# Performance work log

Hardware: AMD Instinct MI355X
Metric: run time of the kernel (lower is better)

Reference implementation:

```python
import jax, jax.numpy as jnp
import numpy as np
from jax import lax

HEADS = 8
DIM_HEAD = 64
DIM = HEADS * DIM_HEAD  # 512


def _dwconv(x_nchw, w):
    # depthwise 3x3, stride 1, pad 1 (SAME), groups = channels
    return lax.conv_general_dilated(
        x_nchw, w, window_strides=(1, 1), padding='SAME',
        feature_group_count=x_nchw.shape[1],
        dimension_numbers=('NCHW', 'OIHW', 'NCHW'))


def setup_inputs() -> dict:
    key = jax.random.key(0)
    ks = jax.random.split(key, 9)
    b, h, w, c = 4, 256, 256, DIM
    s = 1.0 / np.sqrt(c)
    return {
        'x_in':    jax.random.normal(ks[0], (b, h, w, c), jnp.float32),
        'Wq':      jax.random.normal(ks[1], (c, DIM), jnp.float32) * s,
        'Wk':      jax.random.normal(ks[2], (c, DIM), jnp.float32) * s,
        'Wv':      jax.random.normal(ks[3], (c, DIM), jnp.float32) * s,
        'rescale': jnp.ones((HEADS, 1, 1), jnp.float32),
        'proj_w':  jax.random.normal(ks[4], (DIM, c), jnp.float32) * s,
        'proj_b':  jnp.zeros((c,), jnp.float32),
        'conv1_w': jax.random.normal(ks[5], (c, 1, 3, 3), jnp.float32) * (1.0 / 3.0),
        'conv2_w': jax.random.normal(ks[6], (c, 1, 3, 3), jnp.float32) * (1.0 / 3.0),
    }


def reference(x_in, Wq, Wk, Wv, rescale, proj_w, proj_b, conv1_w, conv2_w):
    b, h, w, c = x_in.shape
    n = h * w
    x = x_in.reshape(b, n, c)
    q_inp = x @ Wq  # [b, n, heads*d]
    k_inp = x @ Wk
    v_inp = x @ Wv

    def heads_dn(t):  # [b, n, heads*d] -> [b, heads, d, n]
        return t.reshape(b, n, HEADS, DIM_HEAD).transpose(0, 2, 3, 1)

    q = heads_dn(q_inp)
    k = heads_dn(k_inp)
    v = heads_dn(v_inp)

    # L2-normalize along token axis (F.normalize, eps=1e-12)
    qn = q / jnp.maximum(jnp.linalg.norm(q, axis=-1, keepdims=True), 1e-12)
    kn = k / jnp.maximum(jnp.linalg.norm(k, axis=-1, keepdims=True), 1e-12)

    # channel attention: [b, heads, d, d]
    attn = jnp.einsum('bhdn,bhen->bhde', kn, qn) * rescale
    attn = jax.nn.softmax(attn, axis=-1)
    xo = jnp.einsum('bhde,bhen->bhdn', attn, v)  # [b, heads, d, n]

    xo = xo.transpose(0, 3, 1, 2).reshape(b, n, HEADS * DIM_HEAD)
    out_c = (xo @ proj_w + proj_b).reshape(b, h, w, c)

    # depthwise conv positional embedding on v_inp
    vp = v_inp.reshape(b, h, w, c).transpose(0, 3, 1, 2)  # NCHW
    vp = _dwconv(vp, conv1_w)
    vp = jax.nn.gelu(vp, approximate=False)
    vp = _dwconv(vp, conv2_w)
    out_p = vp.transpose(0, 2, 3, 1)

    return out_c + out_p
```

## Files before the change

kernel.cpp:

```cpp
#include <hip/hip_runtime.h>
#include <math.h>

typedef unsigned short u16;
typedef unsigned int   u32;
typedef __attribute__((ext_vector_type(4))) float f32x4;
typedef __attribute__((ext_vector_type(8))) short bf16x8;
typedef __attribute__((ext_vector_type(8))) u16   u16x8;
typedef __attribute__((ext_vector_type(4))) u16   u16x4;

#define DEVI static __device__ __forceinline__

DEVI float bf2f(u16 a){ u32 u=((u32)a)<<16; float f; __builtin_memcpy(&f,&u,4); return f; }
DEVI u16 f2bf(float f){ u32 u; __builtin_memcpy(&u,&f,4); u=u+0x7fffu+((u>>16)&1u); return (u16)(u>>16); }

DEVI void gload16(const u16* src, u16* lds){
  __builtin_amdgcn_global_load_lds((const __attribute__((address_space(1))) u32*)src,
                                   (__attribute__((address_space(3))) u32*)lds, 16, 0, 0);
}

__global__ void k_wvt(const float* __restrict__ Wv, u16* __restrict__ WvT){
  int n = blockIdx.x;
  for (int k = threadIdx.x; k < 512; k += 256)
    WvT[(size_t)n*512 + k] = f2bf(Wv[(size_t)k*512 + n]);
}
__global__ void k_wrep(const float* __restrict__ w1, const float* __restrict__ w2, float* __restrict__ wt){
  int s = blockIdx.x/9, tap = blockIdx.x%9, c = threadIdx.x;
  const float* w = s ? w2 : w1;
  wt[(size_t)(s*9+tap)*512 + c] = w[(size_t)c*9 + tap];
}

__global__ __launch_bounds__(1024, 4) void k_gemm_v(const float* __restrict__ x, const u16* __restrict__ WvT,
                                                    u16* __restrict__ v, u16* __restrict__ xbT){
  __shared__ __align__(16) u16 Al[128*64];
  __shared__ __align__(16) u16 Bl[512*64];
  const int tid = threadIdx.x;
  const int l = tid & 63, w = tid >> 6;
  const int wr = w >> 3, wc = w & 7;
  const long r0 = (long)blockIdx.x * 128;
  f32x4 acc[4][4] = {};
  const int arow = tid >> 3, ac = tid & 7;
  const float* xp = x + (r0 + arow)*512 + ac*8;
  f32x4 va = *(const f32x4*)xp, vb = *(const f32x4*)(xp+4);
  for (int k0 = 0; k0 < 512; k0 += 64){
    {
      u16x8 o;
      o[0]=f2bf(va.x); o[1]=f2bf(va.y); o[2]=f2bf(va.z); o[3]=f2bf(va.w);
      o[4]=f2bf(vb.x); o[5]=f2bf(vb.y); o[6]=f2bf(vb.z); o[7]=f2bf(vb.w);
      *(u16x8*)&Al[arow*64 + ((ac ^ (arow&7))*8)] = o;
    }
    if (k0 < 448){
      va = *(const f32x4*)(xp + k0 + 64);
      vb = *(const f32x4*)(xp + k0 + 68);
    }
    #pragma unroll
    for (int i = 0; i < 4; ++i){
      int blkrow = w*32 + i*8;
      int r = blkrow + (l>>3);
      const u16* src = WvT + (size_t)r*512 + k0 + (((l&7) ^ ((l>>3)&7))*8);
      gload16(src, &Bl[blkrow*64]);
    }
    __syncthreads();
    #pragma unroll
    for (int ks = 0; ks < 2; ++ks){
      bf16x8 af[4], bfr[4];
      #pragma unroll
      for (int mf = 0; mf < 4; ++mf){
        int row = wr*64 + mf*16 + (l&15);
        af[mf] = *(const bf16x8*)&Al[row*64 + (((ks*4 + (l>>4)) ^ (row&7))*8)];
      }
      #pragma unroll
      for (int nf = 0; nf < 4; ++nf){
        int row = wc*64 + nf*16 + (l&15);
        bfr[nf] = *(const bf16x8*)&Bl[row*64 + (((ks*4 + (l>>4)) ^ (row&7))*8)];
      }
      #pragma unroll
      for (int mf = 0; mf < 4; ++mf)
        #pragma unroll
        for (int nf = 0; nf < 4; ++nf)
          acc[mf][nf] = __builtin_amdgcn_mfma_f32_16x16x32_bf16(af[mf], bfr[nf], acc[mf][nf], 0,0,0);
    }
    {
      int chloc = tid & 63, tg = tid >> 6;
      u16x8 o;
      #pragma unroll
      for (int j = 0; j < 8; ++j){
        int tok = tg*8 + j;
        o[j] = Al[tok*64 + (((chloc>>3) ^ (tok&7))*8) + (chloc&7)];
      }
      *(u16x8*)(xbT + (size_t)(k0 + chloc)*262144 + r0 + tg*8) = o;
    }
    __syncthreads();
  }
  #pragma unroll
  for (int mf = 0; mf < 4; ++mf)
    #pragma unroll
    for (int nf = 0; nf < 4; ++nf){
      int col = wc*64 + nf*16 + (l&15);
      #pragma unroll
      for (int j = 0; j < 4; ++j){
        long row = r0 + wr*64 + mf*16 + (l>>4)*4 + j;
        v[(size_t)row*512 + col] = f2bf(acc[mf][nf][j]);
      }
    }
}

__global__ __launch_bounds__(1024, 4) void k_syrk(const u16* __restrict__ xbT, float* __restrict__ P){
  __shared__ __align__(16) u16 AL[256*64];
  __shared__ __align__(16) u16 BL[256*64];
  const int bid = blockIdx.x;
  const int cs = bid & 63, combo = (bid>>6)%3, b = bid/192;
  const int hA = (combo==2) ? 1 : 0;
  const int tid = threadIdx.x;
  const int l = tid & 63, w = tid>>6, wi = w>>2, wj = w&3;
  const long tokb0 = (long)b*65536 + (long)cs*1024;
  const u16* Bread = (combo==1) ? BL : AL;
  f32x4 acc[4][4] = {};
  for (int st = 0; st < 16; ++st){
    const long tokb = tokb0 + st*64;
    #pragma unroll
    for (int i = 0; i < 2; ++i){
      int blkrow = w*16 + i*8;
      int r = blkrow + (l>>3);
      const u16* src = xbT + (size_t)(hA*256 + r)*262144 + tokb + (((l&7) ^ ((l>>3)&7))*8);
      gload16(src, &AL[blkrow*64]);
    }
    if (combo == 1){
      #pragma unroll
      for (int i = 0; i < 2; ++i){
        int blkrow = w*16 + i*8;
        int r = blkrow + (l>>3);
        const u16* src = xbT + (size_t)(256 + r)*262144 + tokb + (((l&7) ^ ((l>>3)&7))*8);
        gload16(src, &BL[blkrow*64]);
      }
    }
    __syncthreads();
    #pragma unroll
    for (int ks = 0; ks < 2; ++ks){
      bf16x8 af[4], bfr[4];
      #pragma unroll
      for (int mf = 0; mf < 4; ++mf){
        int row = wi*64 + mf*16 + (l&15);
        af[mf] = *(const bf16x8*)&AL[row*64 + (((ks*4 + (l>>4)) ^ (row&7))*8)];
      }
      #pragma unroll
      for (int nf = 0; nf < 4; ++nf){
        int row = wj*64 + nf*16 + (l&15);
        bfr[nf] = *(const bf16x8*)&Bread[row*64 + (((ks*4 + (l>>4)) ^ (row&7))*8)];
      }
      #pragma unroll
      for (int mf = 0; mf < 4; ++mf)
        #pragma unroll
        for (int nf = 0; nf < 4; ++nf)
          acc[mf][nf] = __builtin_amdgcn_mfma_f32_16x16x32_bf16(af[mf], bfr[nf], acc[mf][nf], 0,0,0);
    }
    __syncthreads();
  }
  float* Pb = P + (size_t)bid*65536;
  #pragma unroll
  for (int mf = 0; mf < 4; ++mf)
    #pragma unroll
    for (int nf = 0; nf < 4; ++nf)
      #pragma unroll
      for (int j = 0; j < 4; ++j){
        int il = wi*64 + mf*16 + (l>>4)*4 + j;
        int jl = wj*64 + nf*16 + (l&15);
        Pb[il*256 + jl] = acc[mf][nf][j];
      }
}

__global__ void k_sred(const float* __restrict__ P, float* __restrict__ S){
  int bid = blockIdx.x;
  int il = bid & 255, combo = (bid>>8)%3, b = bid/768;
  int hi = (combo==2)?1:0, hj = (combo==0)?0:1;
  int jl = threadIdx.x;
  float s = 0.f;
  for (int cs = 0; cs < 64; ++cs)
    s += P[((size_t)(b*192 + combo*64 + cs))*65536 + il*256 + jl];
  int I = hi*256 + il, J = hj*256 + jl;
  S[((size_t)b*512 + I)*512 + J] = s;
  if (combo == 1) S[((size_t)b*512 + J)*512 + I] = s;
}

__global__ __launch_bounds__(256) void k_a1(const float* __restrict__ S, const float* __restrict__ Wq,
                                            const float* __restrict__ Wk, float* __restrict__ T, float* __restrict__ U){
  int bid = blockIdx.x;
  int b = bid>>6, rem = bid&63, which = rem>>5, rbase = (rem&31)*16;
  const float* W = which ? Wk : Wq;
  float* O = which ? U : T;
  int tid = threadIdx.x;
  int rg = tid>>6, c0 = (tid&63)*8;
  const float* Sr = S + (size_t)b*262144 + (size_t)(rbase + rg*4)*512;
  float acc[4][8] = {};
  for (int k = 0; k < 512; ++k){
    float s0 = Sr[k], s1 = Sr[512+k], s2 = Sr[1024+k], s3 = Sr[1536+k];
    f32x4 wa = *(const f32x4*)(W + (size_t)k*512 + c0);
    f32x4 wb = *(const f32x4*)(W + (size_t)k*512 + c0 + 4);
    #pragma unroll
    for (int j = 0; j < 4; ++j){
      acc[0][j]   += s0*wa[j]; acc[1][j]   += s1*wa[j]; acc[2][j]   += s2*wa[j]; acc[3][j]   += s3*wa[j];
      acc[0][4+j] += s0*wb[j]; acc[1][4+j] += s1*wb[j]; acc[2][4+j] += s2*wb[j]; acc[3][4+j] += s3*wb[j];
    }
  }
  float* Ob = O + (size_t)b*262144;
  #pragma unroll
  for (int i = 0; i < 4; ++i){
    f32x4 o0, o1;
    o0.x=acc[i][0]; o0.y=acc[i][1]; o0.z=acc[i][2]; o0.w=acc[i][3];
    o1.x=acc[i][4]; o1.y=acc[i][5]; o1.z=acc[i][6]; o1.w=acc[i][7];
    *(f32x4*)(Ob + (size_t)(rbase+rg*4+i)*512 + c0)     = o0;
    *(f32x4*)(Ob + (size_t)(rbase+rg*4+i)*512 + c0 + 4) = o1;
  }
}

__global__ void k_a2(const float* __restrict__ Wq, const float* __restrict__ Wk,
                     const float* __restrict__ T, const float* __restrict__ U,
                     float* __restrict__ G, float* __restrict__ q2, float* __restrict__ k2){
  int b = blockIdx.x>>3, h = blockIdx.x&7;
  int tid = threadIdx.x;
  int d0 = (tid>>4)*4, e0 = (tid&15)*4;
  const float* Tb = T + (size_t)b*262144;
  float acc[4][4] = {};
  for (int i = 0; i < 512; ++i){
    f32x4 wk = *(const f32x4*)(Wk + (size_t)i*512 + h*64 + d0);
    f32x4 tv = *(const f32x4*)(Tb + (size_t)i*512 + h*64 + e0);
    #pragma unroll
    for (int di = 0; di < 4; ++di)
      #pragma unroll
      for (int ej = 0; ej < 4; ++ej) acc[di][ej] += wk[di]*tv[ej];
  }
  float* Gb = G + ((size_t)(b*8+h))*4096;
  #pragma unroll
  for (int di = 0; di < 4; ++di)
    #pragma unroll
    for (int ej = 0; ej < 4; ++ej) Gb[(d0+di)*64 + e0+ej] = acc[di][ej];
  if (tid < 64){
    int e = tid; float a = 0.f;
    for (int j = 0; j < 512; ++j) a += Wq[(size_t)j*512 + h*64 + e] * Tb[(size_t)j*512 + h*64 + e];
    q2[b*512 + h*64 + e] = a;
  } else if (tid < 128){
    int d = tid - 64; float a = 0.f;
    const float* Ub = U + (size_t)b*262144;
    for (int j = 0; j < 512; ++j) a += Wk[(size_t)j*512 + h*64 + d] * Ub[(size_t)j*512 + h*64 + d];
    k2[b*512 + h*64 + d] = a;
  }
}

__global__ void k_a3(const float* __restrict__ G, const float* __restrict__ resc,
                     const float* __restrict__ q2, const float* __restrict__ k2, float* __restrict__ Aa){
  int b = blockIdx.x>>3, h = blockIdx.x&7;
  int d = threadIdx.x;
  const float* g = G + ((size_t)(b*8+h))*4096 + d*64;
  float kn = fmaxf(sqrtf(k2[b*512 + h*64 + d]), 1e-12f);
  float sc = resc[h] / kn;
  float m = -3.4e38f;
  for (int e = 0; e < 64; ++e){
    float qn = fmaxf(sqrtf(q2[b*512 + h*64 + e]), 1e-12f);
    m = fmaxf(m, g[e]*sc/qn);
  }
  float ssum = 0.f;
  for (int e = 0; e < 64; ++e){
    float qn = fmaxf(sqrtf(q2[b*512 + h*64 + e]), 1e-12f);
    ssum += expf(g[e]*sc/qn - m);
  }
  float inv = 1.0f/ssum;
  float* ao = Aa + ((size_t)(b*8+h))*4096 + d*64;
  for (int e = 0; e < 64; ++e){
    float qn = fmaxf(sqrtf(q2[b*512 + h*64 + e]), 1e-12f);
    ao[e] = expf(g[e]*sc/qn - m)*inv;
  }
}

__global__ void k_a4(const float* __restrict__ Aa, const float* __restrict__ pw, u16* __restrict__ MT){
  int bid = blockIdx.x;
  int jt = bid&3, h = (bid>>2)&7, b = bid>>5;
  int tid = threadIdx.x;
  int j = jt*128 + (tid&127), eh = tid>>7;
  const float* Ab = Aa + ((size_t)(b*8+h))*4096;
  float acc[32] = {};
  for (int d = 0; d < 64; ++d){
    float p = pw[(size_t)(h*64+d)*512 + j];
    const float* ar = Ab + d*64 + eh*32;
    #pragma unroll
    for (int q = 0; q < 8; ++q){
      f32x4 pa = *(const f32x4*)(ar + q*4);
      acc[q*4+0] += pa.x*p; acc[q*4+1] += pa.y*p; acc[q*4+2] += pa.z*p; acc[q*4+3] += pa.w*p;
    }
  }
  u16* mo = MT + (size_t)b*262144 + (size_t)j*512 + h*64 + eh*32;
  #pragma unroll
  for (int q = 0; q < 16; ++q){
    u32 pk = (u32)f2bf(acc[2*q]) | ((u32)f2bf(acc[2*q+1])<<16);
    *(u32*)&mo[2*q] = pk;
  }
}

__global__ __launch_bounds__(256) void k_conv1(const u16* __restrict__ v, const float* __restrict__ wt,
                                               u16* __restrict__ t){
  const int logical = (blockIdx.x & 7)*256 + (blockIdx.x >> 3);
  const int xs = logical & 3, yp = (logical>>2) & 127, b = logical >> 9;
  const int tid = threadIdx.x;
  const int ch4 = (tid & 127)*4;
  const int yy = yp*2 + (tid>>7);
  const int x0 = xs*64;
  const u16* vb = v + ((size_t)b*65536)*512 + ch4;
  f32x4 wq[9];
  #pragma unroll
  for (int tap = 0; tap < 9; ++tap) wq[tap] = *(const f32x4*)(wt + (size_t)tap*512 + ch4);
  const bool rok[3] = { yy > 0, true, yy < 255 };

  f32x4 win[3][3];
  #pragma unroll
  for (int r = 0; r < 3; ++r)
    #pragma unroll
    for (int c = 0; c < 2; ++c){
      f32x4 z = {};
      int xx = x0 - 1 + c;
      if (rok[r] && xx >= 0){
        u16x4 raw = *(const u16x4*)(vb + ((size_t)((yy-1+r)*256 + xx))*512);
        z.x=bf2f(raw[0]); z.y=bf2f(raw[1]); z.z=bf2f(raw[2]); z.w=bf2f(raw[3]);
      }
      win[r][c] = z;
    }
  for (int xi = 0; xi < 64; ++xi){
    int x = x0 + xi;
    #pragma unroll
    for (int r = 0; r < 3; ++r){
      f32x4 z = {};
      if (rok[r] && x+1 < 256){
        u16x4 raw = *(const u16x4*)(vb + ((size_t)((yy-1+r)*256 + x+1))*512);
        z.x=bf2f(raw[0]); z.y=bf2f(raw[1]); z.z=bf2f(raw[2]); z.w=bf2f(raw[3]);
      }
      win[r][2] = z;
    }
    u16x4 o;
    #pragma unroll
    for (int j = 0; j < 4; ++j){
      float a = win[0][0][j]*wq[0][j] + win[0][1][j]*wq[1][j] + win[0][2][j]*wq[2][j]
              + win[1][0][j]*wq[3][j] + win[1][1][j]*wq[4][j] + win[1][2][j]*wq[5][j]
              + win[2][0][j]*wq[6][j] + win[2][1][j]*wq[7][j] + win[2][2][j]*wq[8][j];
      float gl = a / (1.0f + __expf(-1.5957691216f*a*(1.0f + 0.044715f*a*a)));
      o[j] = f2bf(gl);
    }
    *(u16x4*)(t + ((size_t)b*65536 + yy*256 + x)*512 + ch4) = o;
    #pragma unroll
    for (int r = 0; r < 3; ++r){ win[r][0] = win[r][1]; win[r][1] = win[r][2]; }
  }
}

__global__ __launch_bounds__(256) void k_conv2(const u16* __restrict__ t, const float* __restrict__ wt,
                                               u16* __restrict__ cbuf){
  const int logical = (blockIdx.x & 7)*256 + (blockIdx.x >> 3);
  const int xs = logical & 3, yp = (logical>>2) & 127, b = logical >> 9;
  const int tid = threadIdx.x;
  const int ch4 = (tid & 127)*4;
  const int yy = yp*2 + (tid>>7);
  const int x0 = xs*64;
  const u16* tb = t + ((size_t)b*65536)*512 + ch4;
  f32x4 wq[9];
  #pragma unroll
  for (int tap = 0; tap < 9; ++tap) wq[tap] = *(const f32x4*)(wt + (size_t)(9+tap)*512 + ch4);
  const bool rok[3] = { yy > 0, true, yy < 255 };

  f32x4 win[3][3];
  #pragma unroll
  for (int r = 0; r < 3; ++r)
    #pragma unroll
    for (int c = 0; c < 2; ++c){
      f32x4 z = {};
      int xx = x0 - 1 + c;
      if (rok[r] && xx >= 0){
        u16x4 raw = *(const u16x4*)(tb + ((size_t)((yy-1+r)*256 + xx))*512);
        z.x=bf2f(raw[0]); z.y=bf2f(raw[1]); z.z=bf2f(raw[2]); z.w=bf2f(raw[3]);
      }
      win[r][c] = z;
    }
  for (int xi = 0; xi < 64; ++xi){
    int x = x0 + xi;
    #pragma unroll
    for (int r = 0; r < 3; ++r){
      f32x4 z = {};
      if (rok[r] && x+1 < 256){
        u16x4 raw = *(const u16x4*)(tb + ((size_t)((yy-1+r)*256 + x+1))*512);
        z.x=bf2f(raw[0]); z.y=bf2f(raw[1]); z.z=bf2f(raw[2]); z.w=bf2f(raw[3]);
      }
      win[r][2] = z;
    }
    u16x4 o;
    #pragma unroll
    for (int j = 0; j < 4; ++j){
      float a = win[0][0][j]*wq[0][j] + win[0][1][j]*wq[1][j] + win[0][2][j]*wq[2][j]
              + win[1][0][j]*wq[3][j] + win[1][1][j]*wq[4][j] + win[1][2][j]*wq[5][j]
              + win[2][0][j]*wq[6][j] + win[2][1][j]*wq[7][j] + win[2][2][j]*wq[8][j];
      o[j] = f2bf(a);
    }
    *(u16x4*)(cbuf + ((size_t)b*65536 + yy*256 + x)*512 + ch4) = o;
    #pragma unroll
    for (int r = 0; r < 3; ++r){ win[r][0] = win[r][1]; win[r][1] = win[r][2]; }
  }
}

__global__ __launch_bounds__(512, 2) void k_gemm_out(const u16* __restrict__ v, const u16* __restrict__ MT,
                                                     const float* __restrict__ proj_b, const u16* __restrict__ cbuf,
                                                     float* __restrict__ out){
  extern __shared__ __align__(16) u16 sm[];
  const int tid = threadIdx.x;
  const int l = tid & 63, w = tid >> 6;
  const int wr = w >> 2, wc = w & 3;
  const int bid = blockIdx.x;
  const int wg = (bid & 7)*256 + (bid >> 3);
  const long r0 = (long)(wg >> 1) * 256;
  const int  c0b = (wg & 1) * 256;
  const int  b = (int)(r0 >> 16);
  const u16* Mb = MT + (size_t)b*262144;
  f32x4 acc[8][4] = {};

  auto STAGE = [&](int buf, int k0){
    u16* Ab = sm + buf*16384;
    u16* Bb = sm + 32768 + buf*16384;
    #pragma unroll
    for (int i = 0; i < 4; ++i){
      int blkrow = w*32 + i*8;
      int r = blkrow + (l>>3);
      gload16(v + (size_t)(r0 + r)*512 + k0 + (((l&7) ^ (r&7))*8), Ab + blkrow*64);
    }
    #pragma unroll
    for (int i = 0; i < 4; ++i){
      int blkrow = w*32 + i*8;
      int r = blkrow + (l>>3);
      gload16(Mb + (size_t)(c0b + r)*512 + k0 + (((l&7) ^ (r&7))*8), Bb + blkrow*64);
    }
  };

  STAGE(0, 0);
  __syncthreads();
  for (int t = 0; t < 8; ++t){
    const int cur = t & 1;
    if (t < 7) STAGE(cur^1, (t+1)*64);
    const u16* Al = sm + cur*16384;
    const u16* Bl = sm + 32768 + cur*16384;
    #pragma unroll
    for (int ks = 0; ks < 2; ++ks){
      bf16x8 bfr[4];
      #pragma unroll
      for (int nf = 0; nf < 4; ++nf){
        int row = wc*64 + nf*16 + (l&15);
        bfr[nf] = *(const bf16x8*)&Bl[row*64 + (((ks*4 + (l>>4)) ^ (row&7))*8)];
      }
      #pragma unroll
      for (int mf = 0; mf < 8; ++mf){
        int row = wr*128 + mf*16 + (l&15);
        bf16x8 af = *(const bf16x8*)&Al[row*64 + (((ks*4 + (l>>4)) ^ (row&7))*8)];
        #pragma unroll
        for (int nf = 0; nf < 4; ++nf)
          acc[mf][nf] = __builtin_amdgcn_mfma_f32_16x16x32_bf16(af, bfr[nf], acc[mf][nf], 0,0,0);
      }
    }
    __syncthreads();
  }
  #pragma unroll
  for (int mf = 0; mf < 8; ++mf)
    #pragma unroll
    for (int nf = 0; nf < 4; ++nf){
      int col = c0b + wc*64 + nf*16 + (l&15);
      float pb = proj_b[col];
      #pragma unroll
      for (int j = 0; j < 4; ++j){
        long row = r0 + wr*128 + mf*16 + (l>>4)*4 + j;
        out[(size_t)row*512 + col] = acc[mf][nf][j] + pb + bf2f(cbuf[(size_t)row*512 + col]);
      }
    }
}

extern "C" void kernel_launch(void* const* d_in, const int* in_sizes, int n_in,
                              void* d_out, int out_size, void* d_ws, size_t ws_size,
                              hipStream_t stream){
  const float* x   = (const float*)d_in[0];
  const float* Wq  = (const float*)d_in[1];
  const float* Wk  = (const float*)d_in[2];
  const float* Wv  = (const float*)d_in[3];
  const float* rsc = (const float*)d_in[4];
  const float* pw  = (const float*)d_in[5];
  const float* pb  = (const float*)d_in[6];
  const float* w1  = (const float*)d_in[7];
  const float* w2  = (const float*)d_in[8];
  float* out = (float*)d_out;
  char* ws = (char*)d_ws;

  const size_t MB256 = 268435456;
  u16*   v    = (u16*)ws;
  u16*   xbT  = (u16*)(ws + MB256);
  u16*   cbuf = xbT;
  char*  sm0  = ws + 2*MB256;
  float* P    = (float*)d_out;
  u16*   t    = (u16*)d_out;

  float* S   = (float*)(sm0);
  float* Tm  = (float*)(sm0 + 4194304);
  float* Um  = (float*)(sm0 + 8388608);
  float* G   = (float*)(sm0 + 12582912);
  float* Aa  = (float*)(sm0 + 13107200);
  float* q2  = (float*)(sm0 + 13631488);
  float* k2  = (float*)(sm0 + 13639680);
  u16*   MT  = (u16*)  (sm0 + 13647872);
  u16*   WvT = (u16*)  (sm0 + 15745024);
  float* wt  = (float*)(sm0 + 16269312);

  k_wvt <<<512, 256, 0, stream>>>(Wv, WvT);
  k_wrep<<<18, 512, 0, stream>>>(w1, w2, wt);
  k_gemm_v<<<2048, 1024, 0, stream>>>(x, WvT, v, xbT);
  k_syrk<<<768, 1024, 0, stream>>>(xbT, P);
  k_sred<<<3072, 256, 0, stream>>>(P, S);
  k_a1<<<256, 256, 0, stream>>>(S, Wq, Wk, Tm, Um);
  k_a2<<<32, 256, 0, stream>>>(Wq, Wk, Tm, Um, G, q2, k2);
  k_a3<<<32, 64, 0, stream>>>(G, rsc, q2, k2, Aa);
  k_a4<<<128, 256, 0, stream>>>(Aa, pw, MT);
  k_conv1<<<2048, 256, 0, stream>>>(v, wt, t);
  k_conv2<<<2048, 256, 0, stream>>>(t, wt, cbuf);
  k_gemm_out<<<2048, 512, 131072, stream>>>(v, MT, pb, cbuf, out);
}
```

Baseline: 1.692 ms.

## Fuse the two depthwise convolutions through shared-memory tiles with halo recompute

Replaces the separate conv1 (with GELU) and conv2 kernels with one kernel. Each block computes a 16-channel, 18x66 conv1+GELU tile into LDS, including a recomputed halo, then runs conv2 from LDS and writes only the final result. This removes the global write and reread of the full bf16 intermediate tensor. In exchange it adds halo recompute, narrower 32-byte channel accesses per pixel, uneven work across threads in the first phase, and LDS pressure that limits occupancy.

```diff
diff --git a/kernel.cpp b/kernel.cpp
--- a/kernel.cpp
+++ b/kernel.cpp
@@ -294,108 +294,109 @@
   }
 }
 
-__global__ __launch_bounds__(256) void k_conv1(const u16* __restrict__ v, const float* __restrict__ wt,
-                                               u16* __restrict__ t){
-  const int logical = (blockIdx.x & 7)*256 + (blockIdx.x >> 3);
-  const int xs = logical & 3, yp = (logical>>2) & 127, b = logical >> 9;
+__global__ __launch_bounds__(256) void k_conv_fused2(const u16* __restrict__ v, const float* __restrict__ wt,
+                                                     u16* __restrict__ cbuf){
+  __shared__ u16 t1[18*69*16];
+  const int logical = (blockIdx.x & 7)*1024 + (blockIdx.x >> 3);
+  const int cg = logical & 31, xs = (logical>>5)&3, ys = (logical>>7)&15, b = logical>>11;
+  const int c0 = cg*16, y0 = ys*16, x0 = xs*64;
   const int tid = threadIdx.x;
-  const int ch4 = (tid & 127)*4;
-  const int yy = yp*2 + (tid>>7);
-  const int x0 = xs*64;
-  const u16* vb = v + ((size_t)b*65536)*512 + ch4;
+  const int quad = tid & 3;
+  const int wkr = tid >> 2;
+  const u16* vb = v + (size_t)b*65536*512 + c0 + quad*4;
+
   f32x4 wq[9];
   #pragma unroll
-  for (int tap = 0; tap < 9; ++tap) wq[tap] = *(const f32x4*)(wt + (size_t)tap*512 + ch4);
-  const bool rok[3] = { yy > 0, true, yy < 255 };
-
-  f32x4 win[3][3];
-  #pragma unroll
-  for (int r = 0; r < 3; ++r)
-    #pragma unroll
-    for (int c = 0; c < 2; ++c){
-      f32x4 z = {};
-      int xx = x0 - 1 + c;
-      if (rok[r] && xx >= 0){
-        u16x4 raw = *(const u16x4*)(vb + ((size_t)((yy-1+r)*256 + xx))*512);
-        z.x=bf2f(raw[0]); z.y=bf2f(raw[1]); z.z=bf2f(raw[2]); z.w=bf2f(raw[3]);
-      }
-      win[r][c] = z;
-    }
-  for (int xi = 0; xi < 64; ++xi){
-    int x = x0 + xi;
-    #pragma unroll
-    for (int r = 0; r < 3; ++r){
-      f32x4 z = {};
-      if (rok[r] && x+1 < 256){
-        u16x4 raw = *(const u16x4*)(vb + ((size_t)((yy-1+r)*256 + x+1))*512);
-        z.x=bf2f(raw[0]); z.y=bf2f(raw[1]); z.z=bf2f(raw[2]); z.w=bf2f(raw[3]);
-      }
-      win[r][2] = z;
-    }
-    u16x4 o;
-    #pragma unroll
-    for (int j = 0; j < 4; ++j){
-      float a = win[0][0][j]*wq[0][j] + win[0][1][j]*wq[1][j] + win[0][2][j]*wq[2][j]
-              + win[1][0][j]*wq[3][j] + win[1][1][j]*wq[4][j] + win[1][2][j]*wq[5][j]
-              + win[2][0][j]*wq[6][j] + win[2][1][j]*wq[7][j] + win[2][2][j]*wq[8][j];
-      float gl = a / (1.0f + __expf(-1.5957691216f*a*(1.0f + 0.044715f*a*a)));
-      o[j] = f2bf(gl);
-    }
-    *(u16x4*)(t + ((size_t)b*65536 + yy*256 + x)*512 + ch4) = o;
-    #pragma unroll
-    for (int r = 0; r < 3; ++r){ win[r][0] = win[r][1]; win[r][1] = win[r][2]; }
-  }
-}
-
-__global__ __launch_bounds__(256) void k_conv2(const u16* __restrict__ t, const float* __restrict__ wt,
-                                               u16* __restrict__ cbuf){
-  const int logical = (blockIdx.x & 7)*256 + (blockIdx.x >> 3);
-  const int xs = logical & 3, yp = (logical>>2) & 127, b = logical >> 9;
-  const int tid = threadIdx.x;
-  const int ch4 = (tid & 127)*4;
-  const int yy = yp*2 + (tid>>7);
-  const int x0 = xs*64;
-  const u16* tb = t + ((size_t)b*65536)*512 + ch4;
-  f32x4 wq[9];
-  #pragma unroll
-  for (int tap = 0; tap < 9; ++tap) wq[tap] = *(const f32x4*)(wt + (size_t)(9+tap)*512 + ch4);
-  const bool rok[3] = { yy > 0, true, yy < 255 };
-
-  f32x4 win[3][3];
-  #pragma unroll
-  for (int r = 0; r < 3; ++r)
-    #pragma unroll
-    for (int c = 0; c < 2; ++c){
-      f32x4 z = {};
-      int xx = x0 - 1 + c;
-      if (rok[r] && xx >= 0){
-        u16x4 raw = *(const u16x4*)(tb + ((size_t)((yy-1+r)*256 + xx))*512);
-        z.x=bf2f(raw[0]); z.y=bf2f(raw[1]); z.z=bf2f(raw[2]); z.w=bf2f(raw[3]);
-      }
-      win[r][c] = z;
-    }
-  for (int xi = 0; xi < 64; ++xi){
-    int x = x0 + xi;
-    #pragma unroll
-    for (int r = 0; r < 3; ++r){
-      f32x4 z = {};
-      if (rok[r] && x+1 < 256){
-        u16x4 raw = *(const u16x4*)(tb + ((size_t)((yy-1+r)*256 + x+1))*512);
-        z.x=bf2f(raw[0]); z.y=bf2f(raw[1]); z.z=bf2f(raw[2]); z.w=bf2f(raw[3]);
-      }
-      win[r][2] = z;
-    }
-    u16x4 o;
-    #pragma unroll
-    for (int j = 0; j < 4; ++j){
-      float a = win[0][0][j]*wq[0][j] + win[0][1][j]*wq[1][j] + win[0][2][j]*wq[2][j]
-              + win[1][0][j]*wq[3][j] + win[1][1][j]*wq[4][j] + win[1][2][j]*wq[5][j]
-              + win[2][0][j]*wq[6][j] + win[2][1][j]*wq[7][j] + win[2][2][j]*wq[8][j];
-      o[j] = f2bf(a);
-    }
-    *(u16x4*)(cbuf + ((size_t)b*65536 + yy*256 + x)*512 + ch4) = o;
-    #pragma unroll
-    for (int r = 0; r < 3; ++r){ win[r][0] = win[r][1]; win[r][1] = win[r][2]; }
+  for (int tap = 0; tap < 9; ++tap)
+    wq[tap] = *(const f32x4*)(wt + (size_t)tap*512 + c0 + quad*4);
+
+  for (int u = wkr; u < 72; u += 64){
+    const int r = u >> 2, xc = u & 3;
+    const int gy = y0 - 1 + r;
+    const int lx0 = xc*17;
+    const int lxe = (lx0 + 17 < 66) ? lx0 + 17 : 66;
+    const bool rowok = (gy >= 0) && (gy < 256);
+    bool yok[3];
+    #pragma unroll
+    for (int rr = 0; rr < 3; ++rr){ int gyr = gy - 1 + rr; yok[rr] = (gyr >= 0) && (gyr < 256); }
+    f32x4 win[3][3];
+    #pragma unroll
+    for (int rr = 0; rr < 3; ++rr)
+      #pragma unroll
+      for (int cc = 0; cc < 2; ++cc){
+        f32x4 z = {};
+        int gx = x0 - 2 + lx0 + cc;
+        if (yok[rr] && gx >= 0 && gx < 256){
+          u16x4 raw = *(const u16x4*)(vb + ((size_t)((gy-1+rr)*256 + gx))*512);
+          z.x=bf2f(raw[0]); z.y=bf2f(raw[1]); z.z=bf2f(raw[2]); z.w=bf2f(raw[3]);
+        }
+        win[rr][cc] = z;
+      }
+    for (int lx = lx0; lx < lxe; ++lx){
+      int gxr = x0 + lx;
+      #pragma unroll
+      for (int rr = 0; rr < 3; ++rr){
+        f32x4 z = {};
+        if (yok[rr] && gxr < 256){
+          u16x4 raw = *(const u16x4*)(vb + ((size_t)((gy-1+rr)*256 + gxr))*512);
+          z.x=bf2f(raw[0]); z.y=bf2f(raw[1]); z.z=bf2f(raw[2]); z.w=bf2f(raw[3]);
+        }
+        win[rr][2] = z;
+      }
+      int gxo = x0 - 1 + lx;
+      bool ok = rowok && (gxo >= 0) && (gxo < 256);
+      u16x4 o;
+      #pragma unroll
+      for (int j = 0; j < 4; ++j){
+        float a = win[0][0][j]*wq[0][j] + win[0][1][j]*wq[1][j] + win[0][2][j]*wq[2][j]
+                + win[1][0][j]*wq[3][j] + win[1][1][j]*wq[4][j] + win[1][2][j]*wq[5][j]
+                + win[2][0][j]*wq[6][j] + win[2][1][j]*wq[7][j] + win[2][2][j]*wq[8][j];
+        float gl = a / (1.0f + __expf(-1.5957691216f*a*(1.0f + 0.044715f*a*a)));
+        o[j] = ok ? f2bf(gl) : (u16)0;
+      }
+      *(u16x4*)&t1[(r*69 + lx)*16 + quad*4] = o;
+      #pragma unroll
+      for (int rr = 0; rr < 3; ++rr){ win[rr][0] = win[rr][1]; win[rr][1] = win[rr][2]; }
+    }
+  }
+
+  #pragma unroll
+  for (int tap = 0; tap < 9; ++tap)
+    wq[tap] = *(const f32x4*)(wt + (size_t)(9+tap)*512 + c0 + quad*4);
+  __syncthreads();
+
+  {
+    const int ro = tid >> 4;
+    const int xc2 = (tid >> 2) & 3;
+    const int gy2 = y0 + ro;
+    f32x4 win[3][3];
+    #pragma unroll
+    for (int rr = 0; rr < 3; ++rr)
+      #pragma unroll
+      for (int cc = 0; cc < 2; ++cc){
+        u16x4 raw = *(const u16x4*)&t1[((ro+rr)*69 + xc2*16 + cc)*16 + quad*4];
+        f32x4 z; z.x=bf2f(raw[0]); z.y=bf2f(raw[1]); z.z=bf2f(raw[2]); z.w=bf2f(raw[3]);
+        win[rr][cc] = z;
+      }
+    for (int i = 0; i < 16; ++i){
+      #pragma unroll
+      for (int rr = 0; rr < 3; ++rr){
+        u16x4 raw = *(const u16x4*)&t1[((ro+rr)*69 + xc2*16 + i + 2)*16 + quad*4];
+        f32x4 z; z.x=bf2f(raw[0]); z.y=bf2f(raw[1]); z.z=bf2f(raw[2]); z.w=bf2f(raw[3]);
+        win[rr][2] = z;
+      }
+      u16x4 o;
+      #pragma unroll
+      for (int j = 0; j < 4; ++j){
+        float a = win[0][0][j]*wq[0][j] + win[0][1][j]*wq[1][j] + win[0][2][j]*wq[2][j]
+                + win[1][0][j]*wq[3][j] + win[1][1][j]*wq[4][j] + win[1][2][j]*wq[5][j]
+                + win[2][0][j]*wq[6][j] + win[2][1][j]*wq[7][j] + win[2][2][j]*wq[8][j];
+        o[j] = f2bf(a);
+      }
+      *(u16x4*)(cbuf + ((size_t)b*65536 + (size_t)gy2*256 + x0 + xc2*16 + i)*512 + c0 + quad*4) = o;
+      #pragma unroll
+      for (int rr = 0; rr < 3; ++rr){ win[rr][0] = win[rr][1]; win[rr][1] = win[rr][2]; }
+    }
   }
 }
 
@@ -492,7 +493,6 @@
   u16*   cbuf = xbT;
   char*  sm0  = ws + 2*MB256;
   float* P    = (float*)d_out;
-  u16*   t    = (u16*)d_out;
 
   float* S   = (float*)(sm0);
   float* Tm  = (float*)(sm0 + 4194304);
@@ -514,7 +514,6 @@
   k_a2<<<32, 256, 0, stream>>>(Wq, Wk, Tm, Um, G, q2, k2);
   k_a3<<<32, 64, 0, stream>>>(G, rsc, q2, k2, Aa);
   k_a4<<<128, 256, 0, stream>>>(Aa, pw, MT);
-  k_conv1<<<2048, 256, 0, stream>>>(v, wt, t);
-  k_conv2<<<2048, 256, 0, stream>>>(t, wt, cbuf);
+  k_conv_fused2<<<8192, 256, 0, stream>>>(v, wt, cbuf);
   k_gemm_out<<<2048, 512, 131072, stream>>>(v, MT, pb, cbuf, out);
 }
```

After: 1.738 ms. 1.03x slower.
